# Kernel tuning notes

Hardware: AMD Instinct MI355X
Metric: run time of the kernel (lower is better)

The kernel has to match this reference:

```python
import jax, jax.numpy as jnp
import numpy as np

B, C, H, W = 8, 256, 64, 64
GROUPS = 32
EPS = 1e-6


def setup_inputs() -> dict:
    key = jax.random.key(0)
    ks = jax.random.split(key, 8)
    s = 0.02
    return {
        "x": jax.random.normal(ks[0], (B, C, H, W), dtype=jnp.float32),
        "gn_scale": jnp.ones((C,), jnp.float32),
        "gn_bias": jnp.zeros((C,), jnp.float32),
        "wq": jax.random.normal(ks[1], (C, C), jnp.float32) * s,
        "bq": jnp.zeros((C,), jnp.float32),
        "wk": jax.random.normal(ks[2], (C, C), jnp.float32) * s,
        "bk": jnp.zeros((C,), jnp.float32),
        "wv": jax.random.normal(ks[3], (C, C), jnp.float32) * s,
        "bv": jnp.zeros((C,), jnp.float32),
        "wproj": jax.random.normal(ks[4], (C, C), jnp.float32) * s,
        "bproj": jnp.zeros((C,), jnp.float32),
    }


def _group_norm(x, scale, bias):
    b, c, h, w = x.shape
    xg = x.reshape(b, GROUPS, c // GROUPS, h, w)
    mean = xg.mean(axis=(2, 3, 4), keepdims=True)
    var = xg.var(axis=(2, 3, 4), keepdims=True)
    xn = ((xg - mean) * jax.lax.rsqrt(var + EPS)).reshape(b, c, h, w)
    return xn * scale[None, :, None, None] + bias[None, :, None, None]


def _conv1x1(x, w, b):
    # 1x1 conv == channel-mixing matmul: w is [out_ch, in_ch]
    return jnp.einsum("oc,bchw->bohw", w, x) + b[None, :, None, None]


def reference(x, gn_scale, gn_bias, wq, bq, wk, bk, wv, bv, wproj, bproj):
    b, c, h, w = x.shape
    hn = _group_norm(x, gn_scale, gn_bias)
    q = _conv1x1(hn, wq, bq).reshape(b, c, h * w)  # [b,c,n]
    k = _conv1x1(hn, wk, bk).reshape(b, c, h * w)
    v = _conv1x1(hn, wv, bv).reshape(b, c, h * w)
    # scores[b,n,m] = <q[:, :, n], k[:, :, m]> * c^-0.5  (softmax over keys m)
    scale = jnp.asarray(c, x.dtype) ** -0.5
    attn = jax.nn.softmax(jnp.einsum("bcn,bcm->bnm", q, k) * scale, axis=2)
    # h_[b,c,n] = sum_m v[b,c,m] * attn[b,n,m]
    h_ = jnp.einsum("bcm,bnm->bcn", v, attn).reshape(b, c, h, w)
    h_ = _conv1x1(h_, wproj, bproj)
    return x + h_
```

## Files before the change

### kernel.cpp

```cpp
#include <hip/hip_runtime.h>

#define B_ 8
#define C_ 256
#define N_ 4096
#define G_ 32

typedef __bf16 bf16;
typedef __bf16 bf16x8 __attribute__((ext_vector_type(8)));
typedef float f32x4 __attribute__((ext_vector_type(4)));
typedef float f32x16 __attribute__((ext_vector_type(16)));
typedef long i64;
typedef long i64x2 __attribute__((ext_vector_type(2)));
typedef long i64x2a __attribute__((ext_vector_type(2), may_alias));
typedef int i32x8 __attribute__((ext_vector_type(8)));
typedef int i32x8a __attribute__((ext_vector_type(8), may_alias));
typedef unsigned int u32;
typedef unsigned char u8;
typedef unsigned short u16;
typedef unsigned long long u64;

__device__ __forceinline__ f32x4 mfma16(bf16x8 a, bf16x8 b, f32x4 c) {
    return __builtin_amdgcn_mfma_f32_16x16x32_bf16(a, b, c, 0, 0, 0);
}
__device__ __forceinline__ f32x16 mfma_mx(i32x8 a, i32x8 b, f32x16 c) {
    return __builtin_amdgcn_mfma_scale_f32_32x32x64_f8f6f4(
        a, b, c, 0 , 0 , 0, 0x7F7F7F7F, 0, 0x7F7F7F7F);
}

typedef __attribute__((address_space(1))) const void* gas_t;
typedef __attribute__((address_space(3))) void* las_t;
__device__ __forceinline__ void gl2lds16(const void* g, void* l) {
    __builtin_amdgcn_global_load_lds((gas_t)g, (las_t)l, 16, 0, 0);
}

__device__ __forceinline__ u32 f32_to_fp8(float x) {
    union { float f; u32 u; } c;
    c.f = x;
    u32 s = (c.u >> 24) & 0x80;
    u32 m = (c.u & 0x7fffffff) + 0x00080000;
    int e = (int)(m >> 23) - 127;
    if (e < -6) return s;
    if (e > 8) return s | 0x7e;
    u32 v = ((u32)(e + 7) << 3) | ((m >> 20) & 7);
    if (v > 0x7e) v = 0x7e;
    return s | v;
}
__device__ __forceinline__ u32 fp8_fast(float x) {
    union { float f; u32 u; } c;
    c.f = x;
    return ((c.u + 0x00080000u) >> 20) - 960u;
}

__global__ __launch_bounds__(256) void gn_stats(const float* __restrict__ x,
                                                float* __restrict__ gstats) {
    int blk = blockIdx.x;
    int b = blk >> 5, g = blk & 31;
    int tid = threadIdx.x;
    int c = g * 8 + (tid >> 5);
    const float* row = x + ((size_t)(b * C_ + c)) * N_;
    float s = 0.f, s2 = 0.f;
    for (int n = (tid & 31) * 4; n < N_; n += 128) {
        float4 v = *(const float4*)(row + n);
        s += v.x + v.y + v.z + v.w;
        s2 += v.x * v.x + v.y * v.y + v.z * v.z + v.w * v.w;
    }
    for (int off = 32; off; off >>= 1) {
        s += __shfl_xor(s, off);
        s2 += __shfl_xor(s2, off);
    }
    __shared__ float red[8];
    int wid = tid >> 6;
    if ((tid & 63) == 0) { red[wid] = s; red[4 + wid] = s2; }
    __syncthreads();
    if (tid == 0) {
        float S = red[0] + red[1] + red[2] + red[3];
        float S2 = red[4] + red[5] + red[6] + red[7];
        float mean = S * (1.f / 32768.f);
        float var = S2 * (1.f / 32768.f) - mean * mean;
        gstats[blk * 2] = mean;
        gstats[blk * 2 + 1] = rsqrtf(var + 1e-6f);
    }
}

__global__ __launch_bounds__(256) void gn_apply(const float* __restrict__ x,
                                                const float* __restrict__ gsc,
                                                const float* __restrict__ gbi,
                                                const float* __restrict__ gstats,
                                                bf16* __restrict__ hn) {
    __shared__ float tile[32][33];
    int b = blockIdx.z, c0 = blockIdx.y * 32, n0 = blockIdx.x * 32;
    int tx = threadIdx.x & 31, ty = threadIdx.x >> 5;
    for (int i = 0; i < 4; i++) {
        int cl = ty + i * 8;
        int c = c0 + cl;
        int g = c >> 3;
        float mean = gstats[(b * G_ + g) * 2];
        float rstd = gstats[(b * G_ + g) * 2 + 1];
        float sc = gsc[c] * rstd;
        float bs = gbi[c] - mean * sc;
        float v = x[((size_t)(b * C_ + c)) * N_ + n0 + tx];
        tile[cl][tx] = v * sc + bs;
    }
    __syncthreads();
    for (int i = 0; i < 4; i++) {
        int nl = ty + i * 8;
        hn[((size_t)(b * N_ + n0 + nl)) * C_ + c0 + tx] = (bf16)tile[tx][nl];
    }
}

__global__ __launch_bounds__(256) void cvt_w(const float* __restrict__ wq,
                                             const float* __restrict__ wk,
                                             const float* __restrict__ wv,
                                             const float* __restrict__ wp,
                                             bf16* __restrict__ dst) {
    int i = blockIdx.x * 256 + threadIdx.x;
    dst[i] = (bf16)wq[i];
    dst[65536 + i] = (bf16)wk[i];
    dst[131072 + i] = (bf16)wv[i];
    dst[196608 + i] = (bf16)wp[i];
}

__global__ __launch_bounds__(256) void gemm_qkv(const bf16* __restrict__ A,
                                                const bf16* __restrict__ Wq,
                                                const bf16* __restrict__ Wk,
                                                const bf16* __restrict__ Wv,
                                                const float* __restrict__ bq,
                                                const float* __restrict__ bk,
                                                const float* __restrict__ bv,
                                                u8* __restrict__ q8,
                                                u8* __restrict__ k8,
                                                u8* __restrict__ v8) {
    __shared__ __align__(16) bf16 As[64][32];
    __shared__ __align__(16) bf16 Wqs[64][32];
    __shared__ __align__(16) bf16 Wks[64][32];
    __shared__ __align__(16) bf16 Wvs[64][32];
    int m0 = blockIdx.x * 64;
    int n0 = blockIdx.y * 64;
    int tid = threadIdx.x;
    int wv_ = tid >> 6, lane = tid & 63, lr = lane & 15, lq = lane >> 4;
    int wm = (wv_ & 1) * 32, wn = (wv_ >> 1) * 32;
    int sr = tid >> 2, sk = (tid & 3) * 8;
    f32x4 qacc[2][2] = {}, kacc[2][2] = {}, vacc[2][2] = {};
    for (int kk = 0; kk < C_; kk += 32) {
        __syncthreads();
        gl2lds16(&A[(size_t)(m0 + sr) * C_ + kk + sk], &As[sr][sk]);
        gl2lds16(&Wq[(size_t)(n0 + sr) * C_ + kk + sk], &Wqs[sr][sk]);
        gl2lds16(&Wk[(size_t)(n0 + sr) * C_ + kk + sk], &Wks[sr][sk]);
        gl2lds16(&Wv[(size_t)(n0 + sr) * C_ + kk + sk], &Wvs[sr][sk]);
        __syncthreads();
        bf16x8 a0 = *(const bf16x8*)&As[wm + lr][lq * 8];
        bf16x8 a1 = *(const bf16x8*)&As[wm + 16 + lr][lq * 8];
        bf16x8 q0 = *(const bf16x8*)&Wqs[wn + lr][lq * 8];
        bf16x8 q1 = *(const bf16x8*)&Wqs[wn + 16 + lr][lq * 8];
        bf16x8 k0 = *(const bf16x8*)&Wks[wn + lr][lq * 8];
        bf16x8 k1 = *(const bf16x8*)&Wks[wn + 16 + lr][lq * 8];
        bf16x8 v0 = *(const bf16x8*)&Wvs[wn + lr][lq * 8];
        bf16x8 v1 = *(const bf16x8*)&Wvs[wn + 16 + lr][lq * 8];
        qacc[0][0] = mfma16(a0, q0, qacc[0][0]);
        qacc[0][1] = mfma16(a0, q1, qacc[0][1]);
        qacc[1][0] = mfma16(a1, q0, qacc[1][0]);
        qacc[1][1] = mfma16(a1, q1, qacc[1][1]);
        kacc[0][0] = mfma16(a0, k0, kacc[0][0]);
        kacc[0][1] = mfma16(a0, k1, kacc[0][1]);
        kacc[1][0] = mfma16(a1, k0, kacc[1][0]);
        kacc[1][1] = mfma16(a1, k1, kacc[1][1]);
        vacc[0][0] = mfma16(a0, v0, vacc[0][0]);
        vacc[0][1] = mfma16(a0, v1, vacc[0][1]);
        vacc[1][0] = mfma16(a1, v0, vacc[1][0]);
        vacc[1][1] = mfma16(a1, v1, vacc[1][1]);
    }
    for (int i = 0; i < 2; i++)
        for (int j = 0; j < 2; j++) {
            int col = n0 + wn + j * 16 + lr;
            float bvq = bq[col], bvk = bk[col], bvv = bv[col];
            for (int r = 0; r < 4; r++) {
                int row = m0 + wm + i * 16 + lq * 4 + r;
                q8[(size_t)row * C_ + col] = (u8)f32_to_fp8(qacc[i][j][r] + bvq);
                k8[(size_t)row * C_ + col] = (u8)f32_to_fp8(kacc[i][j][r] + bvk);
                int bb = row >> 12, n = row & (N_ - 1);
                int h = (n >> 11) & 1, mtl = (n >> 6) & 31, k6 = n & 63;
                int hbv = (k6 >> 2) & 1;
                int jv = ((k6 >> 5) << 4) | (((k6 >> 3) & 3) << 2) | (k6 & 3);
                jv ^= ((col ^ hbv) & 1) << 4;
                v8[((size_t)(((bb * 2 + h) * 32 + mtl) * 2 + hbv)) * 8192 +
                   col * 32 + jv] = (u8)f32_to_fp8(vacc[i][j][r] + bvv);
            }
        }
}

__global__ __launch_bounds__(128, 2) void attn(const u8* __restrict__ q,
                                               const u8* __restrict__ k,
                                               const u8* __restrict__ vT,
                                               bf16* __restrict__ O0,
                                               bf16* __restrict__ O1,
                                               float* __restrict__ lp) {
    __shared__ __align__(16) u8 smem[40960];

    int flat = blockIdx.x + (blockIdx.y << 6) + (blockIdx.z << 7);
    int nid = (flat & 7) * 128 + (flat >> 3);
    int q0 = (nid & 63) * 64;
    int h = (nid >> 6) & 1;
    int b = nid >> 7;
    int tid = threadIdx.x;
    int w = tid >> 6, lane = tid & 63, lc = lane & 31, hb = lane >> 5;

    const u8* kglob = k + ((size_t)(b * N_) + h * 2048) * 256;
    const u8* vglob = vT + ((size_t)(b * 2 + h)) * 32 * 16384;

    u32 offK[4];
#pragma unroll
    for (int j = 0; j < 4; j++) {
        int p = j * 128 + tid;
        offK[j] = (u32)((p >> 4) * 256 + (((p & 15) ^ ((p >> 4) & 15)) << 4));
    }

    const u8* qrow = q + ((size_t)(b * N_ + q0 + w * 32 + lc)) * 256 + hb * 32;
    i32x8 qf[4];
#pragma unroll
    for (int kh = 0; kh < 4; kh++) qf[kh] = *(const i32x8a*)&qrow[kh * 64];

    f32x16 oacc[8] = {};
    float li = 0.f;
    u32 swz = (u32)(lc & 15);
    u32 vsw0 = (u32)(((lc ^ hb) & 1) << 4);

    auto STAGE_K = [&](int sidx, int buf) {
        const u8* kg = kglob + (size_t)sidx * 8192;
        u8* dst = smem + buf * 8192;
#pragma unroll
        for (int j = 0; j < 4; j++)
            gl2lds16(kg + offK[j], dst + (j * 128 + tid) * 16);
    };
    auto STAGE_V = [&](int t) {
        const u8* vg = vglob + (size_t)t * 16384;
#pragma unroll
        for (int j = 0; j < 8; j++)
            gl2lds16(vg + (j * 128 + tid) * 16, smem + 24576 + (j * 128 + tid) * 16);
    };

    STAGE_K(0, 0);
    STAGE_K(1, 1);
    STAGE_V(0);

    for (int mt = 0; mt < 32; mt++) {
        int bufa = (2 * mt) % 3, bufb = (2 * mt + 1) % 3, bufc = (2 * mt + 2) % 3;
        if (mt < 31) {
            STAGE_K(2 * mt + 2, bufc);
            asm volatile("s_waitcnt vmcnt(4)" ::: "memory");
        } else {
            asm volatile("s_waitcnt vmcnt(0)" ::: "memory");
        }
        __builtin_amdgcn_s_barrier();

        const u8* Ka = smem + bufa * 8192;
        const u8* Kb = smem + bufb * 8192;
        __builtin_amdgcn_s_setprio(1);

        f32x16 st0 = {}, st1 = {};
#pragma unroll
        for (int kh = 0; kh < 4; kh++) {
            u32 g0 = (u32)(kh * 4 + hb * 2);
            union { i64x2 h2[2]; i32x8 v; } kf0, kf1;
            kf0.h2[0] = *(const i64x2a*)&Ka[lc * 256 + ((g0 ^ swz) << 4)];
            kf0.h2[1] = *(const i64x2a*)&Ka[lc * 256 + (((g0 + 1) ^ swz) << 4)];
            st0 = mfma_mx(kf0.v, qf[kh], st0);
            kf1.h2[0] = *(const i64x2a*)&Kb[lc * 256 + ((g0 ^ swz) << 4)];
            kf1.h2[1] = *(const i64x2a*)&Kb[lc * 256 + (((g0 + 1) ^ swz) << 4)];
            st1 = mfma_mx(kf1.v, qf[kh], st1);
        }

        i32x8 pf;
#pragma unroll
        for (int t4 = 0; t4 < 4; t4++) {
            float a0 = __expf(st0[t4 * 4 + 0] * 0.0625f);
            float a1 = __expf(st0[t4 * 4 + 1] * 0.0625f);
            float a2 = __expf(st0[t4 * 4 + 2] * 0.0625f);
            float a3 = __expf(st0[t4 * 4 + 3] * 0.0625f);
            float b0 = __expf(st1[t4 * 4 + 0] * 0.0625f);
            float b1 = __expf(st1[t4 * 4 + 1] * 0.0625f);
            float b2 = __expf(st1[t4 * 4 + 2] * 0.0625f);
            float b3 = __expf(st1[t4 * 4 + 3] * 0.0625f);
            li += ((a0 + a1) + (a2 + a3)) + ((b0 + b1) + (b2 + b3));
            pf[t4] = (int)((fp8_fast(a0) & 0xff) | ((fp8_fast(a1) & 0xff) << 8) |
                           ((fp8_fast(a2) & 0xff) << 16) | (fp8_fast(a3) << 24));
            pf[4 + t4] = (int)((fp8_fast(b0) & 0xff) | ((fp8_fast(b1) & 0xff) << 8) |
                               ((fp8_fast(b2) & 0xff) << 16) | (fp8_fast(b3) << 24));
        }

        const u8* Vb = smem + 24576;
#pragma unroll
        for (int ct = 0; ct < 8; ct++) {
            u32 base = (u32)(hb * 8192 + (ct * 32 + lc) * 32);
            union { i64x2 h2[2]; i32x8 v; } vf;
            vf.h2[0] = *(const i64x2a*)&Vb[base + vsw0];
            vf.h2[1] = *(const i64x2a*)&Vb[base + (vsw0 ^ 16)];
            oacc[ct] = mfma_mx(pf, vf.v, oacc[ct]);
        }
        __builtin_amdgcn_s_setprio(0);

        if (mt < 31) {
            asm volatile("s_waitcnt lgkmcnt(0)" ::: "memory");
            __builtin_amdgcn_s_barrier();
            STAGE_K(2 * mt + 3, bufa);
            STAGE_V(mt + 1);
        }
    }

    float lsum = li + __shfl_xor(li, 32);

    bf16* Op = h ? O1 : O0;
#pragma unroll
    for (int ct = 0; ct < 8; ct++)
#pragma unroll
        for (int r = 0; r < 16; r++) {
            int qq = (r & 3) + hb * 4 + (r >> 2) * 8;
            Op[((size_t)(b * N_ + q0 + w * 32 + qq)) * C_ + ct * 32 + lc] =
                (bf16)oacc[ct][r];
        }
    if (hb == 0)
        lp[((size_t)(h * B_ + b)) * N_ + q0 + w * 32 + lc] = lsum;
}

__global__ __launch_bounds__(256) void proj_res(const bf16* __restrict__ W,
                                                const bf16* __restrict__ O0,
                                                const bf16* __restrict__ O1,
                                                const float* __restrict__ lp,
                                                const float* __restrict__ bias,
                                                const float* __restrict__ x,
                                                float* __restrict__ out) {
    __shared__ __align__(16) bf16 Ws[64][32];
    __shared__ __align__(16) bf16 As[64][32];
    int m0 = blockIdx.x * 64;
    int n0 = blockIdx.y * 64;
    int tid = threadIdx.x;
    int wv_ = tid >> 6, lane = tid & 63, lr = lane & 15, lq = lane >> 4;
    int wm = (wv_ & 1) * 32, wn = (wv_ >> 1) * 32;
    int sr = tid >> 2, sk = (tid & 3) * 8;
    int T = n0 + sr, bb = T >> 12, nn = T & (N_ - 1);
    float inv = 1.f / (lp[(size_t)bb * N_ + nn] + lp[(size_t)(B_ + bb) * N_ + nn]);
    f32x4 acc[2][2] = {};
    for (int kk = 0; kk < C_; kk += 32) {
        __syncthreads();
        gl2lds16(&W[(size_t)(m0 + sr) * C_ + kk + sk], &Ws[sr][sk]);
        bf16x8 o0 = *(const bf16x8*)&O0[(size_t)T * C_ + kk + sk];
        bf16x8 o1 = *(const bf16x8*)&O1[(size_t)T * C_ + kk + sk];
        bf16x8 cm;
#pragma unroll
        for (int e = 0; e < 8; e++) cm[e] = (bf16)(((float)o0[e] + (float)o1[e]) * inv);
        *(bf16x8*)&As[sr][sk] = cm;
        __syncthreads();
        bf16x8 a0 = *(const bf16x8*)&Ws[wm + lr][lq * 8];
        bf16x8 a1 = *(const bf16x8*)&Ws[wm + 16 + lr][lq * 8];
        bf16x8 b0 = *(const bf16x8*)&As[wn + lr][lq * 8];
        bf16x8 b1 = *(const bf16x8*)&As[wn + 16 + lr][lq * 8];
        acc[0][0] = mfma16(a0, b0, acc[0][0]);
        acc[0][1] = mfma16(a0, b1, acc[0][1]);
        acc[1][0] = mfma16(a1, b0, acc[1][0]);
        acc[1][1] = mfma16(a1, b1, acc[1][1]);
    }
    for (int i = 0; i < 2; i++)
        for (int j = 0; j < 2; j++) {
            int Tt = n0 + wn + j * 16 + lr;
            int b = Tt >> 12, n = Tt & (N_ - 1);
            for (int r = 0; r < 4; r++) {
                int o = m0 + wm + i * 16 + lq * 4 + r;
                size_t idx = ((size_t)(b * C_ + o)) * N_ + n;
                out[idx] = x[idx] + acc[i][j][r] + bias[o];
            }
        }
}

extern "C" void kernel_launch(void* const* d_in, const int* in_sizes, int n_in,
                              void* d_out, int out_size, void* d_ws, size_t ws_size,
                              hipStream_t stream) {
    const float* x = (const float*)d_in[0];
    const float* gsc = (const float*)d_in[1];
    const float* gbi = (const float*)d_in[2];
    const float* wq = (const float*)d_in[3];
    const float* bq = (const float*)d_in[4];
    const float* wk = (const float*)d_in[5];
    const float* bk = (const float*)d_in[6];
    const float* wv = (const float*)d_in[7];
    const float* bv = (const float*)d_in[8];
    const float* wp = (const float*)d_in[9];
    const float* bp = (const float*)d_in[10];
    float* out = (float*)d_out;

    const size_t SZ = (size_t)B_ * N_ * C_;
    char* ws = (char*)d_ws;
    float* gstats = (float*)ws;
    bf16* wb = (bf16*)(ws + 4096);
    char* base = ws + 4096 + 524288;
    bf16* hn = (bf16*)base;
    u8* q8 = (u8*)(base + SZ * 2);
    u8* k8 = (u8*)(base + SZ * 3);
    u8* v8 = (u8*)(base + SZ * 4);
    bf16* O0 = (bf16*)base;
    bf16* O1 = (bf16*)(base + SZ * 5);
    float* lpart = (float*)(base + SZ * 7);

    cvt_w<<<256, 256, 0, stream>>>(wq, wk, wv, wp, wb);
    gn_stats<<<B_ * G_, 256, 0, stream>>>(x, gstats);
    gn_apply<<<dim3(N_ / 32, C_ / 32, B_), 256, 0, stream>>>(x, gsc, gbi, gstats, hn);
    gemm_qkv<<<dim3(B_ * N_ / 64, C_ / 64), 256, 0, stream>>>(
        hn, wb, wb + 65536, wb + 131072, bq, bk, bv, q8, k8, v8);
    attn<<<dim3(N_ / 64, 2, B_), 128, 0, stream>>>(q8, k8, v8, O0, O1, lpart);
    proj_res<<<dim3(C_ / 64, B_ * N_ / 64), 256, 0, stream>>>(
        wb + 196608, O0, O1, lpart, bp, x, out);
}
```

Measured before the change: 278.1 us.

## Split GN stats across more blocks, use hardware exp2/fp8 pack, widen proj tile

Group-norm statistics are now computed as 8 partial sums per group across 2048 blocks, and gn_apply reduces them, which raises parallelism for the stats pass. The attention softmax uses the hardware exp2 instruction and the packed fp8 conversion builtin, and keeps the row sum in a vector accumulator. proj_res now computes all 256 output channels per block, so each token tile's O0/O1 combine is done once instead of four times, at the cost of more accumulator registers and LDS. gpart aliases lpart, which is safe only because gn_apply finishes before attn writes lpart.

```diff
diff --git a/kernel.cpp b/kernel.cpp
--- a/kernel.cpp
+++ b/kernel.cpp
@@ -33,6 +33,10 @@
     __builtin_amdgcn_global_load_lds((gas_t)g, (las_t)l, 16, 0, 0);
 }
 
+__device__ __forceinline__ float exp2_hw(float x) {
+    return __builtin_amdgcn_exp2f(x);
+}
+
 __device__ __forceinline__ u32 f32_to_fp8(float x) {
     union { float f; u32 u; } c;
     c.f = x;
@@ -50,16 +54,26 @@
     c.f = x;
     return ((c.u + 0x00080000u) >> 20) - 960u;
 }
-
-__global__ __launch_bounds__(256) void gn_stats(const float* __restrict__ x,
-                                                float* __restrict__ gstats) {
+__device__ __forceinline__ u32 pk_fp8x4(float a, float b, float c, float d) {
+#if __has_builtin(__builtin_amdgcn_cvt_pk_fp8_f32)
+    int w = __builtin_amdgcn_cvt_pk_fp8_f32(a, b, 0, false);
+    w = __builtin_amdgcn_cvt_pk_fp8_f32(c, d, w, true);
+    return (u32)w;
+#else
+    return (fp8_fast(a) & 0xff) | ((fp8_fast(b) & 0xff) << 8) |
+           ((fp8_fast(c) & 0xff) << 16) | (fp8_fast(d) << 24);
+#endif
+}
+
+__global__ __launch_bounds__(256) void gn_part(const float* __restrict__ x,
+                                               float* __restrict__ gpart) {
     int blk = blockIdx.x;
-    int b = blk >> 5, g = blk & 31;
+    int b = blk >> 8, g = (blk >> 3) & 31, qe = blk & 7;
     int tid = threadIdx.x;
     int c = g * 8 + (tid >> 5);
-    const float* row = x + ((size_t)(b * C_ + c)) * N_;
+    const float* row = x + ((size_t)(b * C_ + c)) * N_ + qe * 512;
     float s = 0.f, s2 = 0.f;
-    for (int n = (tid & 31) * 4; n < N_; n += 128) {
+    for (int n = (tid & 31) * 4; n < 512; n += 128) {
         float4 v = *(const float4*)(row + n);
         s += v.x + v.y + v.z + v.w;
         s2 += v.x * v.x + v.y * v.y + v.z * v.z + v.w * v.w;
@@ -73,19 +87,15 @@
     if ((tid & 63) == 0) { red[wid] = s; red[4 + wid] = s2; }
     __syncthreads();
     if (tid == 0) {
-        float S = red[0] + red[1] + red[2] + red[3];
-        float S2 = red[4] + red[5] + red[6] + red[7];
-        float mean = S * (1.f / 32768.f);
-        float var = S2 * (1.f / 32768.f) - mean * mean;
-        gstats[blk * 2] = mean;
-        gstats[blk * 2 + 1] = rsqrtf(var + 1e-6f);
+        gpart[blk * 2] = red[0] + red[1] + red[2] + red[3];
+        gpart[blk * 2 + 1] = red[4] + red[5] + red[6] + red[7];
     }
 }
 
 __global__ __launch_bounds__(256) void gn_apply(const float* __restrict__ x,
                                                 const float* __restrict__ gsc,
                                                 const float* __restrict__ gbi,
-                                                const float* __restrict__ gstats,
+                                                const float* __restrict__ gpart,
                                                 bf16* __restrict__ hn) {
     __shared__ float tile[32][33];
     int b = blockIdx.z, c0 = blockIdx.y * 32, n0 = blockIdx.x * 32;
@@ -94,8 +104,13 @@
         int cl = ty + i * 8;
         int c = c0 + cl;
         int g = c >> 3;
-        float mean = gstats[(b * G_ + g) * 2];
-        float rstd = gstats[(b * G_ + g) * 2 + 1];
+        const float* gp = gpart + ((size_t)(b * G_ + g)) * 16;
+        float S = 0.f, S2 = 0.f;
+#pragma unroll
+        for (int j = 0; j < 8; j++) { S += gp[j * 2]; S2 += gp[j * 2 + 1]; }
+        float mean = S * (1.f / 32768.f);
+        float var = S2 * (1.f / 32768.f) - mean * mean;
+        float rstd = rsqrtf(var + 1e-6f);
         float sc = gsc[c] * rstd;
         float bs = gbi[c] - mean * sc;
         float v = x[((size_t)(b * C_ + c)) * N_ + n0 + tx];
@@ -220,7 +235,7 @@
     for (int kh = 0; kh < 4; kh++) qf[kh] = *(const i32x8a*)&qrow[kh * 64];
 
     f32x16 oacc[8] = {};
-    float li = 0.f;
+    f32x16 eacc = {};
     u32 swz = (u32)(lc & 15);
     u32 vsw0 = (u32)(((lc ^ hb) & 1) << 4);
 
@@ -269,22 +284,21 @@
             st1 = mfma_mx(kf1.v, qf[kh], st1);
         }
 
+        f32x16 e0, e1;
+#pragma unroll
+        for (int i = 0; i < 16; i++) {
+            e0[i] = exp2_hw(st0[i] * (1.44269504089f * 0.0625f));
+            e1[i] = exp2_hw(st1[i] * (1.44269504089f * 0.0625f));
+        }
+        eacc += e0;
+        eacc += e1;
         i32x8 pf;
 #pragma unroll
         for (int t4 = 0; t4 < 4; t4++) {
-            float a0 = __expf(st0[t4 * 4 + 0] * 0.0625f);
-            float a1 = __expf(st0[t4 * 4 + 1] * 0.0625f);
-            float a2 = __expf(st0[t4 * 4 + 2] * 0.0625f);
-            float a3 = __expf(st0[t4 * 4 + 3] * 0.0625f);
-            float b0 = __expf(st1[t4 * 4 + 0] * 0.0625f);
-            float b1 = __expf(st1[t4 * 4 + 1] * 0.0625f);
-            float b2 = __expf(st1[t4 * 4 + 2] * 0.0625f);
-            float b3 = __expf(st1[t4 * 4 + 3] * 0.0625f);
-            li += ((a0 + a1) + (a2 + a3)) + ((b0 + b1) + (b2 + b3));
-            pf[t4] = (int)((fp8_fast(a0) & 0xff) | ((fp8_fast(a1) & 0xff) << 8) |
-                           ((fp8_fast(a2) & 0xff) << 16) | (fp8_fast(a3) << 24));
-            pf[4 + t4] = (int)((fp8_fast(b0) & 0xff) | ((fp8_fast(b1) & 0xff) << 8) |
-                               ((fp8_fast(b2) & 0xff) << 16) | (fp8_fast(b3) << 24));
+            pf[t4] = (int)pk_fp8x4(e0[t4 * 4], e0[t4 * 4 + 1], e0[t4 * 4 + 2],
+                                   e0[t4 * 4 + 3]);
+            pf[4 + t4] = (int)pk_fp8x4(e1[t4 * 4], e1[t4 * 4 + 1], e1[t4 * 4 + 2],
+                                       e1[t4 * 4 + 3]);
         }
 
         const u8* Vb = smem + 24576;
@@ -306,7 +320,10 @@
         }
     }
 
-    float lsum = li + __shfl_xor(li, 32);
+    float hs = 0.f;
+#pragma unroll
+    for (int i = 0; i < 16; i++) hs += eacc[i];
+    float lsum = hs + __shfl_xor(hs, 32);
 
     bf16* Op = h ? O1 : O0;
 #pragma unroll
@@ -328,20 +345,22 @@
                                                 const float* __restrict__ bias,
                                                 const float* __restrict__ x,
                                                 float* __restrict__ out) {
-    __shared__ __align__(16) bf16 Ws[64][32];
+    __shared__ __align__(16) bf16 Ws[256][32];
     __shared__ __align__(16) bf16 As[64][32];
-    int m0 = blockIdx.x * 64;
-    int n0 = blockIdx.y * 64;
+    int n0 = blockIdx.x * 64;
     int tid = threadIdx.x;
     int wv_ = tid >> 6, lane = tid & 63, lr = lane & 15, lq = lane >> 4;
-    int wm = (wv_ & 1) * 32, wn = (wv_ >> 1) * 32;
+    int wm = (wv_ & 1) * 32;
+    int wn = (wv_ >> 1) * 32;
     int sr = tid >> 2, sk = (tid & 3) * 8;
     int T = n0 + sr, bb = T >> 12, nn = T & (N_ - 1);
     float inv = 1.f / (lp[(size_t)bb * N_ + nn] + lp[(size_t)(B_ + bb) * N_ + nn]);
-    f32x4 acc[2][2] = {};
+    f32x4 acc[4][2][2] = {};
     for (int kk = 0; kk < C_; kk += 32) {
         __syncthreads();
-        gl2lds16(&W[(size_t)(m0 + sr) * C_ + kk + sk], &Ws[sr][sk]);
+#pragma unroll
+        for (int p = 0; p < 4; p++)
+            gl2lds16(&W[(size_t)(p * 64 + sr) * C_ + kk + sk], &Ws[p * 64 + sr][sk]);
         bf16x8 o0 = *(const bf16x8*)&O0[(size_t)T * C_ + kk + sk];
         bf16x8 o1 = *(const bf16x8*)&O1[(size_t)T * C_ + kk + sk];
         bf16x8 cm;
@@ -349,25 +368,30 @@
         for (int e = 0; e < 8; e++) cm[e] = (bf16)(((float)o0[e] + (float)o1[e]) * inv);
         *(bf16x8*)&As[sr][sk] = cm;
         __syncthreads();
-        bf16x8 a0 = *(const bf16x8*)&Ws[wm + lr][lq * 8];
-        bf16x8 a1 = *(const bf16x8*)&Ws[wm + 16 + lr][lq * 8];
-        bf16x8 b0 = *(const bf16x8*)&As[wn + lr][lq * 8];
-        bf16x8 b1 = *(const bf16x8*)&As[wn + 16 + lr][lq * 8];
-        acc[0][0] = mfma16(a0, b0, acc[0][0]);
-        acc[0][1] = mfma16(a0, b1, acc[0][1]);
-        acc[1][0] = mfma16(a1, b0, acc[1][0]);
-        acc[1][1] = mfma16(a1, b1, acc[1][1]);
-    }
-    for (int i = 0; i < 2; i++)
-        for (int j = 0; j < 2; j++) {
-            int Tt = n0 + wn + j * 16 + lr;
-            int b = Tt >> 12, n = Tt & (N_ - 1);
-            for (int r = 0; r < 4; r++) {
-                int o = m0 + wm + i * 16 + lq * 4 + r;
-                size_t idx = ((size_t)(b * C_ + o)) * N_ + n;
-                out[idx] = x[idx] + acc[i][j][r] + bias[o];
+        bf16x8 a0 = *(const bf16x8*)&As[wm + lr][lq * 8];
+        bf16x8 a1 = *(const bf16x8*)&As[wm + 16 + lr][lq * 8];
+#pragma unroll
+        for (int ot = 0; ot < 4; ot++) {
+            bf16x8 w0 = *(const bf16x8*)&Ws[ot * 64 + wn + lr][lq * 8];
+            bf16x8 w1 = *(const bf16x8*)&Ws[ot * 64 + wn + 16 + lr][lq * 8];
+            acc[ot][0][0] = mfma16(w0, a0, acc[ot][0][0]);
+            acc[ot][0][1] = mfma16(w0, a1, acc[ot][0][1]);
+            acc[ot][1][0] = mfma16(w1, a0, acc[ot][1][0]);
+            acc[ot][1][1] = mfma16(w1, a1, acc[ot][1][1]);
+        }
+    }
+#pragma unroll
+    for (int ot = 0; ot < 4; ot++)
+        for (int i = 0; i < 2; i++)
+            for (int j = 0; j < 2; j++) {
+                int Tt = n0 + wm + j * 16 + lr;
+                int b = Tt >> 12, n = Tt & (N_ - 1);
+                for (int r = 0; r < 4; r++) {
+                    int o = ot * 64 + wn + i * 16 + lq * 4 + r;
+                    size_t idx = ((size_t)(b * C_ + o)) * N_ + n;
+                    out[idx] = x[idx] + acc[ot][i][j][r] + bias[o];
+                }
             }
-        }
 }
 
 extern "C" void kernel_launch(void* const* d_in, const int* in_sizes, int n_in,
@@ -388,7 +412,6 @@
 
     const size_t SZ = (size_t)B_ * N_ * C_;
     char* ws = (char*)d_ws;
-    float* gstats = (float*)ws;
     bf16* wb = (bf16*)(ws + 4096);
     char* base = ws + 4096 + 524288;
     bf16* hn = (bf16*)base;
@@ -397,14 +420,15 @@
     u8* v8 = (u8*)(base + SZ * 4);
     bf16* O0 = (bf16*)base;
     bf16* O1 = (bf16*)(base + SZ * 5);
+    float* gpart = (float*)(base + SZ * 7);
     float* lpart = (float*)(base + SZ * 7);
 
     cvt_w<<<256, 256, 0, stream>>>(wq, wk, wv, wp, wb);
-    gn_stats<<<B_ * G_, 256, 0, stream>>>(x, gstats);
-    gn_apply<<<dim3(N_ / 32, C_ / 32, B_), 256, 0, stream>>>(x, gsc, gbi, gstats, hn);
+    gn_part<<<B_ * G_ * 8, 256, 0, stream>>>(x, gpart);
+    gn_apply<<<dim3(N_ / 32, C_ / 32, B_), 256, 0, stream>>>(x, gsc, gbi, gpart, hn);
     gemm_qkv<<<dim3(B_ * N_ / 64, C_ / 64), 256, 0, stream>>>(
         hn, wb, wb + 65536, wb + 131072, bq, bk, bv, q8, k8, v8);
     attn<<<dim3(N_ / 64, 2, B_), 128, 0, stream>>>(q8, k8, v8, O0, O1, lpart);
-    proj_res<<<dim3(C_ / 64, B_ * N_ / 64), 256, 0, stream>>>(
+    proj_res<<<B_ * N_ / 64, 256, 0, stream>>>(
         wb + 196608, O0, O1, lpart, bp, x, out);
 }
```

After: 255.4 us. 8.2% less time.
